# Kernel optimization log

Hardware: AMD Instinct MI355X
Metric: run time of the kernel (lower is better)

Reference implementation:

```python
import jax, jax.numpy as jnp
import numpy as np

B, C, H, W = 8, 256, 64, 64
HEADS, HID = 8, 64
TMP = HEADS * HID  # 512


def setup_inputs() -> dict:
    key = jax.random.key(0)
    ks = jax.random.split(key, 6)
    s = lambda fan: 1.0 / np.sqrt(fan)
    fmap = jax.random.normal(ks[0], (B, C, H, W), jnp.float32)
    Wq = jax.random.normal(ks[1], (TMP, C), jnp.float32) * s(C)          # to_q 1x1 conv (no bias)
    Wdw = jax.random.normal(ks[2], (C, 1, 3, 3), jnp.float32) * s(9)     # depthwise 3x3 (groups=C, no bias)
    Wkv = jax.random.normal(ks[3], (2 * TMP, C), jnp.float32) * s(C)     # 1x1 conv producing k,v (no bias)
    Wout = jax.random.normal(ks[4], (C, TMP), jnp.float32) * s(TMP)      # to_out 1x1 conv
    bout = jax.random.normal(ks[5], (C,), jnp.float32) * 0.01
    return {"fmap": fmap, "Wq": Wq, "Wdw": Wdw, "Wkv": Wkv, "Wout": Wout, "bout": bout}


def reference(fmap, Wq, Wdw, Wkv, Wout, bout):
    heads, hid = HEADS, HID
    scale = hid ** (-0.5)
    b, c, h, w = fmap.shape
    n = h * w

    # 1x1 conv == channel GEMM
    q = jnp.einsum('bcxy,oc->boxy', fmap, Wq)
    # depthwise 3x3, padding=1
    dw = jax.lax.conv_general_dilated(
        fmap, Wdw, window_strides=(1, 1), padding='SAME',
        dimension_numbers=('NCHW', 'OIHW', 'NCHW'), feature_group_count=c)
    kv = jnp.einsum('bcxy,oc->boxy', dw, Wkv)
    k, v = jnp.split(kv, 2, axis=1)

    # 'b (h c) x y -> b h (x y) c'
    def to_seq(t):
        return t.reshape(b, heads, hid, n).transpose(0, 1, 3, 2)  # [b, h, n, d]

    q, k, v = to_seq(q), to_seq(k), to_seq(v)
    q = jax.nn.softmax(q, axis=-1) * scale   # softmax over feature dim
    k = jax.nn.softmax(k, axis=-2)           # softmax over token dim

    ctx = jnp.einsum('bhnd,bhne->bhde', k, v)    # [b, h, d, d]
    out = jnp.einsum('bhnd,bhde->bhne', q, ctx)  # [b, h, n, d]

    # '(b h) (x y) d -> b (h d) x y'
    out = out.transpose(0, 1, 3, 2).reshape(b, heads * hid, h, w)

    # to_out: GELU (exact) then 1x1 conv with bias (mode='ac')
    out = jax.nn.gelu(out, approximate=False)
    return jnp.einsum('bcxy,oc->boxy', out, Wout) + bout[None, :, None, None]
```

## Files before the change

### kernel.cpp

```cpp
#include <hip/hip_runtime.h>
#include <hip/hip_bf16.h>
#include <math.h>

#define Bx 8
#define Cc 256
#define Nn 4096
#define TMPc 512

typedef unsigned short ushort;
typedef unsigned int uint;
typedef unsigned long long ull;
typedef __attribute__((ext_vector_type(8))) short bf16x8;
typedef __attribute__((ext_vector_type(4))) float f32x4;

union F4 { float4 v; float f[4]; };

__device__ __forceinline__ ushort f2bf(float x) {
  uint u = __float_as_uint(x);
  uint r = (u + 0x7fffu + ((u >> 16) & 1u)) >> 16;
  return (ushort)r;
}
__device__ __forceinline__ float gelu_fast(float x) {
  float u = 0.70710678118654752f * x;
  float au = fabsf(u);
  float t = __builtin_amdgcn_rcpf(1.0f + 0.3275911f * au);
  float poly = ((((1.061405429f * t - 1.453152027f) * t + 1.421413741f) * t -
                 0.284496736f) * t + 0.254829592f) * t;
  float e = 1.0f - poly * __expf(-u * u);
  float erfu = copysignf(e, u);
  return 0.5f * x * (1.0f + erfu);
}

typedef const __attribute__((address_space(1))) uint* gp1_t;
typedef __attribute__((address_space(3))) uint* lp3_t;
__device__ __forceinline__ void gload16(void* lds, const void* g) {
  __builtin_amdgcn_global_load_lds((gp1_t)g, (lp3_t)lds, 16, 0, 0);
}
__device__ __forceinline__ void lgkm_fence() {
  asm volatile("s_waitcnt lgkmcnt(0)" ::: "memory");
}
__device__ __forceinline__ bf16x8 fragread(const char* lds, int row, int kc) {
  return *(const bf16x8*)(lds + row * 64 + ((kc ^ (row & 3)) << 4));
}
__device__ __forceinline__ void stage2(char* buf, const ushort* src, int ld,
                                       int row0, int col, int w, int prow, int gst) {
  int off = __builtin_amdgcn_readfirstlane(w * 2048);
  gload16(buf + off, src + (size_t)(row0 + prow) * ld + col + gst * 8);
  gload16(buf + off + 1024, src + (size_t)(row0 + 16 + prow) * ld + col + gst * 8);
}

#define CGRP 32
__global__ __launch_bounds__(256) void convw_k(const float* __restrict__ fmap,
                                               const float* __restrict__ Wdw,
                                               ushort* __restrict__ fmapT,
                                               ushort* __restrict__ dwT,
                                               const float* __restrict__ Wq,
                                               const float* __restrict__ Wkv,
                                               const float* __restrict__ Wout,
                                               ushort* __restrict__ WqB,
                                               ushort* __restrict__ WkvB,
                                               ushort* __restrict__ WoutB) {
  __shared__ float sin_[CGRP][6 * 64 + 1];
  __shared__ float wl[CGRP][9];
  int t = threadIdx.x;
  if (blockIdx.z == 8) {
    int wid = blockIdx.y * 16 + blockIdx.x;
#pragma unroll
    for (int g = 0; g < 4; ++g) {
      int i = wid * 1024 + g * 256 + t;
      const float* s;
      ushort* d;
      int idx;
      if (i < 32768) { s = Wq; d = WqB; idx = i; }
      else if (i < 98304) { s = Wkv; d = WkvB; idx = i - 32768; }
      else { s = Wout; d = WoutB; idx = i - 98304; }
      F4 v; v.v = *(const float4*)&s[(size_t)idx * 4];
      union { ushort u[4]; uint2 q; } o;
#pragma unroll
      for (int j = 0; j < 4; ++j) o.u[j] = f2bf(v.f[j]);
      *(uint2*)&d[(size_t)idx * 4] = o.q;
    }
    return;
  }
  int y0 = blockIdx.x * 4;
  int c0 = blockIdx.y * CGRP;
  int z = blockIdx.z;
  for (int i = t; i < CGRP * 9; i += 256) wl[i / 9][i % 9] = Wdw[c0 * 9 + i];
  const float* src = fmap + ((size_t)z * Cc + c0) * 4096;
#pragma unroll
  for (int it = 0; it < 12; ++it) {
    int idx = it * 256 + t;
    int c = idx / 96, rem = idx % 96, yy = rem >> 4, x4 = rem & 15;
    int gy = y0 - 1 + yy;
    F4 v;
    if ((unsigned)gy < 64u)
      v.v = *(const float4*)&src[(size_t)c * 4096 + gy * 64 + x4 * 4];
    else
      v.f[0] = v.f[1] = v.f[2] = v.f[3] = 0.f;
#pragma unroll
    for (int j = 0; j < 4; ++j) sin_[c][yy * 64 + x4 * 4 + j] = v.f[j];
  }
  __syncthreads();
  int c8 = (t & 3) * 8;
  int x = t >> 2;
  size_t nbase = (size_t)z * 4096 + (size_t)y0 * 64;
  union { ushort u[8]; uint4 q; } fo[4], go[4];
#pragma unroll
  for (int cc = 0; cc < 8; ++cc) {
    int c = c8 + cc;
    float wr[9];
#pragma unroll
    for (int k = 0; k < 9; ++k) wr[k] = wl[c][k];
    float r[6][3];
#pragma unroll
    for (int row = 0; row < 6; ++row) {
      r[row][1] = sin_[c][row * 64 + x];
      r[row][0] = (x > 0) ? sin_[c][row * 64 + x - 1] : 0.f;
      r[row][2] = (x < 63) ? sin_[c][row * 64 + x + 1] : 0.f;
    }
#pragma unroll
    for (int it = 0; it < 4; ++it) {
      fo[it].u[cc] = f2bf(r[it + 1][1]);
      float acc = 0.f;
#pragma unroll
      for (int dy = 0; dy < 3; ++dy)
#pragma unroll
        for (int dx = 0; dx < 3; ++dx)
          acc += r[it + dy][dx] * wr[dy * 3 + dx];
      go[it].u[cc] = f2bf(acc);
    }
  }
#pragma unroll
  for (int it = 0; it < 4; ++it) {
    *(uint4*)&fmapT[(nbase + it * 64 + x) * Cc + c0 + c8] = fo[it].q;
    *(uint4*)&dwT[(nbase + it * 64 + x) * Cc + c0 + c8] = go[it].q;
  }
}

__global__ __launch_bounds__(256, 2) void kvgemm3_k(const ushort* __restrict__ WkvB,
                                                    const ushort* __restrict__ dwT,
                                                    ushort* __restrict__ kv) {
  __shared__ __align__(16) char lds[57344];
  char* Bres = lds;
  char* Asg  = lds + 32768;
  int t = threadIdx.x, w = t >> 6, l = t & 63;
  int z = blockIdx.y, n0 = blockIdx.x * 64;
  int rl = l & 15, kc = l >> 4;
  int prow = l >> 2;
  int gst = (l & 3) ^ ((l >> 2) & 3);

  const ushort* dT = dwT + ((size_t)z * 4096 + n0) * 256;
#pragma unroll
  for (int p = 0; p < 8; ++p) {
    int row = (w * 8 + p) * 2 + (l >> 5);
    int cs = l & 31;
    int off = __builtin_amdgcn_readfirstlane((w * 8 + p) * 1024);
    gload16(Bres + off, dT + (size_t)row * 256 + ((cs ^ (row & 7)) * 8));
  }
  stage2(Asg, WkvB, 256, w * 32, 0, w, prow, gst);
  stage2(Asg + 8192, WkvB, 256, w * 32, 32, w, prow, gst);
  asm volatile("s_waitcnt vmcnt(0)" ::: "memory");
  __syncthreads();

  ushort* kz = kv + (size_t)z * 1024 * 4096;
#pragma unroll
  for (int c = 0; c < 8; ++c) {
    f32x4 acc[2][4];
#pragma unroll
    for (int i = 0; i < 2; ++i)
#pragma unroll
      for (int j = 0; j < 4; ++j) acc[i][j] = (f32x4){0.f, 0.f, 0.f, 0.f};
#pragma unroll
    for (int k0 = 0; k0 < 8; ++k0) {
      int s = c * 8 + k0;
      if (s + 2 < 64) {
        int s2 = s + 2;
        lgkm_fence();
        stage2(Asg + (s2 % 3) * 8192, WkvB, 256, (s2 >> 3) * 128 + w * 32,
               (s2 & 7) * 32, w, prow, gst);
      }
      if (s < 62) asm volatile("s_waitcnt vmcnt(4)" ::: "memory");
      else if (s == 62) asm volatile("s_waitcnt vmcnt(2)" ::: "memory");
      else asm volatile("s_waitcnt vmcnt(0)" ::: "memory");
      const char* bp = Asg + (s % 3) * 8192 + w * 2048;
      bf16x8 a0 = fragread(bp, rl, kc);
      bf16x8 a1 = fragread(bp, 16 + rl, kc);
      __builtin_amdgcn_s_setprio(1);
#pragma unroll
      for (int j = 0; j < 4; ++j) {
        int n = 16 * j + rl;
        bf16x8 b = *(const bf16x8*)(Bres + n * 512 + (((k0 * 4 + kc) ^ (n & 7)) << 4));
        acc[0][j] = __builtin_amdgcn_mfma_f32_16x16x32_bf16(a0, b, acc[0][j], 0, 0, 0);
        acc[1][j] = __builtin_amdgcn_mfma_f32_16x16x32_bf16(a1, b, acc[1][j], 0, 0, 0);
      }
      __builtin_amdgcn_s_setprio(0);
    }
#pragma unroll
    for (int i = 0; i < 2; ++i) {
#pragma unroll
      for (int reg = 0; reg < 4; ++reg) {
        int r = c * 128 + w * 32 + 16 * i + 4 * kc + reg;
#pragma unroll
        for (int j = 0; j < 4; ++j) {
          int col = n0 + 16 * j + rl;
          float v = acc[i][j][reg];
          kz[(size_t)r * 4096 + col] = f2bf(c < 4 ? __expf(v) : v);
        }
      }
    }
  }
}

__global__ __launch_bounds__(256) void ctx_mfma(const ushort* __restrict__ kv,
                                                float* __restrict__ ctxf,
                                                float* __restrict__ sf) {
  __shared__ __align__(16) char lds[16384];
  int t = threadIdx.x, w = t >> 6, l = t & 63;
  int s = blockIdx.x;
  int h = blockIdx.y & 7, z = blockIdx.y >> 3;
  const ushort* kb = kv + ((size_t)z * 1024 + h * 64) * 4096;
  const ushort* vb = kv + ((size_t)z * 1024 + 512 + h * 64) * 4096;
  f32x4 acc[2][2];
  f32x4 accs[2];
#pragma unroll
  for (int i = 0; i < 2; ++i) {
    accs[i] = (f32x4){0.f, 0.f, 0.f, 0.f};
#pragma unroll
    for (int j = 0; j < 2; ++j) acc[i][j] = (f32x4){0.f, 0.f, 0.f, 0.f};
  }
  bf16x8 ones;
#pragma unroll
  for (int i = 0; i < 8; ++i) ones[i] = (short)0x3F80;
  int wr = (w >> 1) * 32, wc = (w & 1) * 32;
  int rl = l & 15, kc = l >> 4;
  int srow = (l >> 2) & 15, scol = l & 3;
  int row = w * 16 + srow;
  int g = scol ^ (row & 3);
  int soff = __builtin_amdgcn_readfirstlane(w * 1024);
#define CSTG(bb, it)                                                      \
  {                                                                       \
    int k0_ = s * 512 + (it) * 32;                                        \
    gload16(lds + (bb) + soff, vb + (size_t)row * 4096 + k0_ + g * 8);    \
    gload16(lds + (bb) + 4096 + soff, kb + (size_t)row * 4096 + k0_ + g * 8); \
  }
  CSTG(0, 0);
  asm volatile("s_waitcnt vmcnt(0)" ::: "memory");
  __syncthreads();
  for (int it = 0; it < 16; ++it) {
    int cur = (it & 1) << 13;
    if (it + 1 < 16) CSTG(cur ^ 8192, it + 1);
    bf16x8 a[2], b[2];
#pragma unroll
    for (int i = 0; i < 2; ++i) a[i] = fragread(lds + cur, wr + i * 16 + rl, kc);
#pragma unroll
    for (int i = 0; i < 2; ++i) b[i] = fragread(lds + cur + 4096, wc + i * 16 + rl, kc);
#pragma unroll
    for (int i = 0; i < 2; ++i)
#pragma unroll
      for (int j = 0; j < 2; ++j)
        acc[i][j] = __builtin_amdgcn_mfma_f32_16x16x32_bf16(a[i], b[j], acc[i][j], 0, 0, 0);
    if (w < 2) {
#pragma unroll
      for (int j = 0; j < 2; ++j)
        accs[j] = __builtin_amdgcn_mfma_f32_16x16x32_bf16(b[j], ones, accs[j], 0, 0, 0);
    }
    asm volatile("s_waitcnt vmcnt(0)" ::: "memory");
    __syncthreads();
  }
  float* cf = ctxf + (size_t)(z * 8 + h) * 4096;
#pragma unroll
  for (int i = 0; i < 2; ++i)
#pragma unroll
    for (int reg = 0; reg < 4; ++reg) {
      int e = wr + i * 16 + kc * 4 + reg;
#pragma unroll
      for (int j = 0; j < 2; ++j) {
        int d = wc + j * 16 + rl;
        atomicAdd(&cf[e * 64 + d], acc[i][j][reg]);
      }
    }
  if (w < 2 && rl == 0) {
    float* sp = sf + (size_t)(z * 8 + h) * 64;
#pragma unroll
    for (int j = 0; j < 2; ++j)
#pragma unroll
      for (int reg = 0; reg < 4; ++reg)
        atomicAdd(&sp[wc + j * 16 + kc * 4 + reg], accs[j][reg]);
  }
#undef CSTG
}

__global__ __launch_bounds__(256) void ctx_cvt(const float* __restrict__ ctxf,
                                               const float* __restrict__ sf,
                                               ushort* __restrict__ ctxb) {
  int page = blockIdx.x;
  const float* s = ctxf + (size_t)page * 4096;
  const float* sp = sf + (size_t)page * 64;
  ushort* d = ctxb + (size_t)page * 4096;
  int t = threadIdx.x;
  int e = t >> 2, d0 = (t & 3) * 16;
  union { ushort u[16]; uint4 q[2]; } o;
#pragma unroll
  for (int j = 0; j < 16; ++j) {
    int dd = d0 + j;
    o.u[j] = f2bf(s[e * 64 + dd] / sp[dd]);
  }
  uint4* dp = (uint4*)&d[e * 64 + d0];
  dp[0] = o.q[0]; dp[1] = o.q[1];
}

__global__ __launch_bounds__(256, 2) void qao_k(const ushort* __restrict__ fmapT,
                                                const ushort* __restrict__ WqB,
                                                const ushort* __restrict__ ctxb,
                                                const ushort* __restrict__ WoutB,
                                                const float* __restrict__ bout,
                                                float* __restrict__ out) {
  __shared__ __align__(16) char lds[73728];
  __shared__ float wsum[4][64];
  char* qbuf = lds;
  char* Bres = lds + 16384;
  char* Asg  = lds + 49152;
  int t = threadIdx.x, w = t >> 6, l = t & 63;
  int z = blockIdx.y, n0 = blockIdx.x * 64;
  int rl = l & 15, kc = l >> 4;
  int prow = l >> 2;
  int gst = (l & 3) ^ ((l >> 2) & 3);
  int hh = w >> 1;
  int wcn = (w & 1) * 32;

  const ushort* fT = fmapT + ((size_t)z * 4096 + n0) * 256;
#pragma unroll
  for (int p = 0; p < 8; ++p) {
    int row = (w * 8 + p) * 2 + (l >> 5);
    int cs = l & 31;
    int off = __builtin_amdgcn_readfirstlane((w * 8 + p) * 1024);
    gload16(Bres + off, fT + (size_t)row * 256 + ((cs ^ (row & 7)) * 8));
  }
  stage2(Asg, WqB, 256, w * 32, 0, w, prow, gst);
  stage2(Asg + 8192, WqB, 256, w * 32, 32, w, prow, gst);

  f32x4 oacc[4][4];
#pragma unroll
  for (int i = 0; i < 4; ++i)
#pragma unroll
    for (int j = 0; j < 4; ++j) oacc[i][j] = (f32x4){0.f, 0.f, 0.f, 0.f};

  asm volatile("s_waitcnt vmcnt(0)" ::: "memory");
  __syncthreads();

  for (int c = 0; c < 4; ++c) {
    const ushort* Wqc = WqB + (size_t)(c * 128) * 256;
    f32x4 qa[2][4];
#pragma unroll
    for (int i = 0; i < 2; ++i)
#pragma unroll
      for (int j = 0; j < 4; ++j) qa[i][j] = (f32x4){0.f, 0.f, 0.f, 0.f};
#pragma unroll
    for (int k0 = 0; k0 < 8; ++k0) {
      if (k0 + 2 < 8) {
        lgkm_fence();
        stage2(Asg + ((k0 + 2) % 3) * 8192, Wqc, 256, w * 32, (k0 + 2) * 32, w, prow, gst);
      }
      if (k0 < 6) asm volatile("s_waitcnt vmcnt(4)" ::: "memory");
      else if (k0 == 6) asm volatile("s_waitcnt vmcnt(2)" ::: "memory");
      else asm volatile("s_waitcnt vmcnt(0)" ::: "memory");
      const char* bp = Asg + (k0 % 3) * 8192 + w * 2048;
      bf16x8 a0 = fragread(bp, rl, kc);
      bf16x8 a1 = fragread(bp, 16 + rl, kc);
      __builtin_amdgcn_s_setprio(1);
#pragma unroll
      for (int j = 0; j < 4; ++j) {
        int n = 16 * j + rl;
        bf16x8 b = *(const bf16x8*)(Bres + n * 512 + (((k0 * 4 + kc) ^ (n & 7)) << 4));
        qa[0][j] = __builtin_amdgcn_mfma_f32_16x16x32_bf16(a0, b, qa[0][j], 0, 0, 0);
        qa[1][j] = __builtin_amdgcn_mfma_f32_16x16x32_bf16(a1, b, qa[1][j], 0, 0, 0);
      }
      __builtin_amdgcn_s_setprio(0);
    }
    const ushort* cpg = ctxb + (size_t)(z * 8 + c * 2 + hh) * 4096;
    bf16x8 ca[2][4];
#pragma unroll
    for (int s2 = 0; s2 < 2; ++s2)
#pragma unroll
      for (int i = 0; i < 4; ++i)
        ca[s2][i] = *(const bf16x8*)(cpg + (size_t)(16 * i + rl) * 64 + s2 * 32 + kc * 8);
    float sj[4];
#pragma unroll
    for (int j = 0; j < 4; ++j) {
      float s = 0.f;
#pragma unroll
      for (int i = 0; i < 2; ++i)
#pragma unroll
        for (int reg = 0; reg < 4; ++reg) {
          float e = __expf(qa[i][j][reg]);
          qa[i][j][reg] = e;
          s += e;
        }
      s += __shfl_xor(s, 16, 64);
      s += __shfl_xor(s, 32, 64);
      sj[j] = s;
    }
    if (l < 16) {
#pragma unroll
      for (int j = 0; j < 4; ++j) wsum[w][j * 16 + l] = sj[j];
    }
    __syncthreads();
#pragma unroll
    for (int j = 0; j < 4; ++j) {
      float tot = wsum[w][16 * j + rl] + wsum[w ^ 1][16 * j + rl];
      float inv = 0.125f / tot;
#pragma unroll
      for (int i = 0; i < 2; ++i)
#pragma unroll
        for (int reg = 0; reg < 4; ++reg) qa[i][j][reg] *= inv;
    }
#pragma unroll
    for (int i = 0; i < 2; ++i)
#pragma unroll
      for (int j = 0; j < 4; ++j) {
        int n = 16 * j + rl;
        int dby = (w * 32 + 16 * i + 4 * kc) * 2;
        union { ushort u[4]; ull q; } pk;
#pragma unroll
        for (int reg = 0; reg < 4; ++reg) pk.u[reg] = f2bf(qa[i][j][reg]);
        *(ull*)(qbuf + n * 256 + (dby ^ ((n & 7) << 4))) = pk.q;
      }
    __syncthreads();
    f32x4 pacc[4][2];
#pragma unroll
    for (int i = 0; i < 4; ++i)
#pragma unroll
      for (int j = 0; j < 2; ++j) pacc[i][j] = (f32x4){0.f, 0.f, 0.f, 0.f};
    __builtin_amdgcn_s_setprio(1);
#pragma unroll
    for (int s2 = 0; s2 < 2; ++s2) {
      bf16x8 pb[2];
#pragma unroll
      for (int j = 0; j < 2; ++j) {
        int n = wcn + 16 * j + rl;
        int dby = hh * 128 + s2 * 64 + kc * 16;
        pb[j] = *(const bf16x8*)(qbuf + n * 256 + (dby ^ ((n & 7) << 4)));
      }
#pragma unroll
      for (int i = 0; i < 4; ++i)
#pragma unroll
        for (int j = 0; j < 2; ++j)
          pacc[i][j] = __builtin_amdgcn_mfma_f32_16x16x32_bf16(ca[s2][i], pb[j], pacc[i][j], 0, 0, 0);
    }
    __builtin_amdgcn_s_setprio(0);
#pragma unroll
    for (int i = 0; i < 4; ++i)
#pragma unroll
      for (int j = 0; j < 2; ++j) {
        int n = wcn + 16 * j + rl;
        int mby = (hh * 64 + 16 * i + 4 * kc) * 2;
        union { ushort u[4]; ull q; } pk;
#pragma unroll
        for (int reg = 0; reg < 4; ++reg) pk.u[reg] = f2bf(gelu_fast(pacc[i][j][reg]));
        *(ull*)(qbuf + n * 256 + (mby ^ ((n & 7) << 4))) = pk.q;
      }
    __syncthreads();
    stage2(Asg, WoutB, 512, w * 64, c * 128, w, prow, gst);
    stage2(Asg + 8192, WoutB, 512, w * 64 + 32, c * 128, w, prow, gst);
    bf16x8 ob[4];
#pragma unroll
    for (int s = 0; s < 8; ++s) {
      if (s + 2 < 8) {
        int s2 = s + 2;
        lgkm_fence();
        stage2(Asg + (s2 % 3) * 8192, WoutB, 512, w * 64 + (s2 & 1) * 32,
               c * 128 + (s2 >> 1) * 32, w, prow, gst);
      }
      if (s < 6) asm volatile("s_waitcnt vmcnt(4)" ::: "memory");
      else if (s == 6) asm volatile("s_waitcnt vmcnt(2)" ::: "memory");
      else asm volatile("s_waitcnt vmcnt(0)" ::: "memory");
      int half = s & 1, ks = s >> 1;
      if (half == 0) {
#pragma unroll
        for (int j = 0; j < 4; ++j) {
          int n = 16 * j + rl;
          ob[j] = *(const bf16x8*)(qbuf + n * 256 + ((ks * 64 + kc * 16) ^ ((n & 7) << 4)));
        }
      }
      const char* bp = Asg + (s % 3) * 8192 + w * 2048;
      bf16x8 a0 = fragread(bp, rl, kc);
      bf16x8 a1 = fragread(bp, 16 + rl, kc);
      __builtin_amdgcn_s_setprio(1);
#pragma unroll
      for (int j = 0; j < 4; ++j) {
        oacc[half * 2][j] = __builtin_amdgcn_mfma_f32_16x16x32_bf16(a0, ob[j], oacc[half * 2][j], 0, 0, 0);
        oacc[half * 2 + 1][j] = __builtin_amdgcn_mfma_f32_16x16x32_bf16(a1, ob[j], oacc[half * 2 + 1][j], 0, 0, 0);
      }
      __builtin_amdgcn_s_setprio(0);
    }
    if (c < 3) {
      const ushort* Wqn = WqB + (size_t)((c + 1) * 128) * 256;
      lgkm_fence();
      stage2(Asg, Wqn, 256, w * 32, 0, w, prow, gst);
      stage2(Asg + 8192, Wqn, 256, w * 32, 32, w, prow, gst);
    }
  }
  float* oz = out + (size_t)z * Cc * Nn + n0;
#pragma unroll
  for (int i = 0; i < 4; ++i) {
#pragma unroll
    for (int reg = 0; reg < 4; ++reg) {
      int crow = w * 64 + 16 * i + 4 * kc + reg;
      float bv = bout[crow];
      float* rowp = oz + (size_t)crow * 4096;
#pragma unroll
      for (int j = 0; j < 4; ++j) rowp[16 * j + rl] = oacc[i][j][reg] + bv;
    }
  }
}

extern "C" void kernel_launch(void* const* d_in, const int* in_sizes, int n_in,
                              void* d_out, int out_size, void* d_ws, size_t ws_size,
                              hipStream_t stream) {
  (void)in_sizes; (void)n_in; (void)out_size; (void)ws_size;
  const float* fmap = (const float*)d_in[0];
  const float* Wq   = (const float*)d_in[1];
  const float* Wdw  = (const float*)d_in[2];
  const float* Wkv  = (const float*)d_in[3];
  const float* Wout = (const float*)d_in[4];
  const float* bout = (const float*)d_in[5];
  float* out = (float*)d_out;

  ushort* WqB   = (ushort*)d_ws;
  ushort* WkvB  = WqB + 512 * 256;
  ushort* WoutB = WkvB + 1024 * 256;
  ushort* fmapT = WoutB + 256 * 512;
  ushort* dwT   = fmapT + (size_t)Bx * 4096 * 256;
  ushort* kv    = dwT + (size_t)Bx * 4096 * 256;
  ushort* ctxb  = kv + (size_t)Bx * 1024 * 4096;
  float*  ctxf  = (float*)(ctxb + (size_t)Bx * 8 * 4096);
  float*  sf    = ctxf + (size_t)Bx * 8 * 64 * 64;

  hipMemsetAsync(ctxf, 0, (size_t)Bx * 8 * (4096 + 64) * sizeof(float), stream);
  convw_k<<<dim3(16, 8, 9), 256, 0, stream>>>(fmap, Wdw, fmapT, dwT,
                                              Wq, Wkv, Wout, WqB, WkvB, WoutB);
  kvgemm3_k<<<dim3(64, Bx), 256, 0, stream>>>(WkvB, dwT, kv);
  ctx_mfma<<<dim3(8, Bx * 8), 256, 0, stream>>>(kv, ctxf, sf);
  ctx_cvt<<<dim3(Bx * 8), 256, 0, stream>>>(ctxf, sf, ctxb);
  qao_k<<<dim3(64, Bx), 256, 0, stream>>>(fmapT, WqB, ctxb, WoutB, bout, out);
}
```

Baseline: 118.9 us.

## Fold memset and ctx conversion into neighbors; shrink kv GEMM staging for occupancy

New measurement: 121.4 us. 1.02x slower.

```diff
diff --git a/kernel.cpp b/kernel.cpp
--- a/kernel.cpp
+++ b/kernel.cpp
@@ -59,12 +59,15 @@
                                                const float* __restrict__ Wout,
                                                ushort* __restrict__ WqB,
                                                ushort* __restrict__ WkvB,
-                                               ushort* __restrict__ WoutB) {
+                                               ushort* __restrict__ WoutB,
+                                               float* __restrict__ ctxf) {
   __shared__ float sin_[CGRP][6 * 64 + 1];
   __shared__ float wl[CGRP][9];
   int t = threadIdx.x;
   if (blockIdx.z == 8) {
     int wid = blockIdx.y * 16 + blockIdx.x;
+    for (int i = wid * 256 + t; i < 66560; i += 32768)
+      *(float4*)&ctxf[(size_t)i * 4] = (float4){0.f, 0.f, 0.f, 0.f};
 #pragma unroll
     for (int g = 0; g < 4; ++g) {
       int i = wid * 1024 + g * 256 + t;
@@ -137,10 +140,10 @@
   }
 }
 
-__global__ __launch_bounds__(256, 2) void kvgemm3_k(const ushort* __restrict__ WkvB,
+__global__ __launch_bounds__(256, 3) void kvgemm3_k(const ushort* __restrict__ WkvB,
                                                     const ushort* __restrict__ dwT,
                                                     ushort* __restrict__ kv) {
-  __shared__ __align__(16) char lds[57344];
+  __shared__ __align__(16) char lds[49152];
   char* Bres = lds;
   char* Asg  = lds + 32768;
   int t = threadIdx.x, w = t >> 6, l = t & 63;
@@ -158,7 +161,6 @@
     gload16(Bres + off, dT + (size_t)row * 256 + ((cs ^ (row & 7)) * 8));
   }
   stage2(Asg, WkvB, 256, w * 32, 0, w, prow, gst);
-  stage2(Asg + 8192, WkvB, 256, w * 32, 32, w, prow, gst);
   asm volatile("s_waitcnt vmcnt(0)" ::: "memory");
   __syncthreads();
 
@@ -173,16 +175,15 @@
 #pragma unroll
     for (int k0 = 0; k0 < 8; ++k0) {
       int s = c * 8 + k0;
-      if (s + 2 < 64) {
-        int s2 = s + 2;
+      if (s + 1 < 64) {
+        int s2 = s + 1;
         lgkm_fence();
-        stage2(Asg + (s2 % 3) * 8192, WkvB, 256, (s2 >> 3) * 128 + w * 32,
+        stage2(Asg + ((s2 & 1) ? 8192 : 0), WkvB, 256, (s2 >> 3) * 128 + w * 32,
                (s2 & 7) * 32, w, prow, gst);
       }
-      if (s < 62) asm volatile("s_waitcnt vmcnt(4)" ::: "memory");
-      else if (s == 62) asm volatile("s_waitcnt vmcnt(2)" ::: "memory");
+      if (s < 63) asm volatile("s_waitcnt vmcnt(2)" ::: "memory");
       else asm volatile("s_waitcnt vmcnt(0)" ::: "memory");
-      const char* bp = Asg + (s % 3) * 8192 + w * 2048;
+      const char* bp = Asg + ((s & 1) ? 8192 : 0) + w * 2048;
       bf16x8 a0 = fragread(bp, rl, kc);
       bf16x8 a1 = fragread(bp, 16 + rl, kc);
       __builtin_amdgcn_s_setprio(1);
@@ -290,28 +291,10 @@
 #undef CSTG
 }
 
-__global__ __launch_bounds__(256) void ctx_cvt(const float* __restrict__ ctxf,
-                                               const float* __restrict__ sf,
-                                               ushort* __restrict__ ctxb) {
-  int page = blockIdx.x;
-  const float* s = ctxf + (size_t)page * 4096;
-  const float* sp = sf + (size_t)page * 64;
-  ushort* d = ctxb + (size_t)page * 4096;
-  int t = threadIdx.x;
-  int e = t >> 2, d0 = (t & 3) * 16;
-  union { ushort u[16]; uint4 q[2]; } o;
-#pragma unroll
-  for (int j = 0; j < 16; ++j) {
-    int dd = d0 + j;
-    o.u[j] = f2bf(s[e * 64 + dd] / sp[dd]);
-  }
-  uint4* dp = (uint4*)&d[e * 64 + d0];
-  dp[0] = o.q[0]; dp[1] = o.q[1];
-}
-
 __global__ __launch_bounds__(256, 2) void qao_k(const ushort* __restrict__ fmapT,
                                                 const ushort* __restrict__ WqB,
-                                                const ushort* __restrict__ ctxb,
+                                                const float* __restrict__ ctxf,
+                                                const float* __restrict__ sf,
                                                 const ushort* __restrict__ WoutB,
                                                 const float* __restrict__ bout,
                                                 float* __restrict__ out) {
@@ -377,13 +360,30 @@
       }
       __builtin_amdgcn_s_setprio(0);
     }
-    const ushort* cpg = ctxb + (size_t)(z * 8 + c * 2 + hh) * 4096;
+    const float* cpgf = ctxf + (size_t)(z * 8 + c * 2 + hh) * 4096;
+    const float* spg  = sf + (size_t)(z * 8 + c * 2 + hh) * 64;
     bf16x8 ca[2][4];
 #pragma unroll
-    for (int s2 = 0; s2 < 2; ++s2)
-#pragma unroll
-      for (int i = 0; i < 4; ++i)
-        ca[s2][i] = *(const bf16x8*)(cpg + (size_t)(16 * i + rl) * 64 + s2 * 32 + kc * 8);
+    for (int s2 = 0; s2 < 2; ++s2) {
+      F4 sv0, sv1;
+      sv0.v = *(const float4*)&spg[s2 * 32 + kc * 8];
+      sv1.v = *(const float4*)&spg[s2 * 32 + kc * 8 + 4];
+      float r0[4], r1[4];
+#pragma unroll
+      for (int m = 0; m < 4; ++m) { r0[m] = 1.0f / sv0.f[m]; r1[m] = 1.0f / sv1.f[m]; }
+#pragma unroll
+      for (int i = 0; i < 4; ++i) {
+        const float* rowp = cpgf + (size_t)(16 * i + rl) * 64 + s2 * 32 + kc * 8;
+        F4 c0, c1;
+        c0.v = *(const float4*)rowp;
+        c1.v = *(const float4*)(rowp + 4);
+#pragma unroll
+        for (int m = 0; m < 4; ++m) {
+          ca[s2][i][m] = (short)f2bf(c0.f[m] * r0[m]);
+          ca[s2][i][4 + m] = (short)f2bf(c1.f[m] * r1[m]);
+        }
+      }
+    }
     float sj[4];
 #pragma unroll
     for (int j = 0; j < 4; ++j) {
@@ -532,15 +532,12 @@
   ushort* fmapT = WoutB + 256 * 512;
   ushort* dwT   = fmapT + (size_t)Bx * 4096 * 256;
   ushort* kv    = dwT + (size_t)Bx * 4096 * 256;
-  ushort* ctxb  = kv + (size_t)Bx * 1024 * 4096;
-  float*  ctxf  = (float*)(ctxb + (size_t)Bx * 8 * 4096);
+  float*  ctxf  = (float*)(kv + (size_t)Bx * 1024 * 4096);
   float*  sf    = ctxf + (size_t)Bx * 8 * 64 * 64;
 
-  hipMemsetAsync(ctxf, 0, (size_t)Bx * 8 * (4096 + 64) * sizeof(float), stream);
   convw_k<<<dim3(16, 8, 9), 256, 0, stream>>>(fmap, Wdw, fmapT, dwT,
-                                              Wq, Wkv, Wout, WqB, WkvB, WoutB);
+                                              Wq, Wkv, Wout, WqB, WkvB, WoutB, ctxf);
   kvgemm3_k<<<dim3(64, Bx), 256, 0, stream>>>(WkvB, dwT, kv);
   ctx_mfma<<<dim3(8, Bx * 8), 256, 0, stream>>>(kv, ctxf, sf);
-  ctx_cvt<<<dim3(Bx * 8), 256, 0, stream>>>(ctxf, sf, ctxb);
-  qao_k<<<dim3(64, Bx), 256, 0, stream>>>(fmapT, WqB, ctxb, WoutB, bout, out);
-}
+  qao_k<<<dim3(64, Bx), 256, 0, stream>>>(fmapT, WqB, ctxf, sf, WoutB, bout, out);
+}
```
